# Kernel tuning notes

Hardware: AMD Instinct MI355X
Metric: run time of the kernel (lower is better)

Reference implementation:

```python
import jax, jax.numpy as jnp
import numpy as np

B, S, D, H = 1, 4096, 1024, 16
HD = D // H  # head_dim = 64
NEG = -1e9

def setup_inputs() -> dict:
    key = jax.random.key(0)
    ks = jax.random.split(key, 5)
    scale = 1.0 / np.sqrt(D)
    x = jax.random.normal(ks[0], (B, S, D), dtype=jnp.float32)
    Wq = jax.random.normal(ks[1], (D, D), dtype=jnp.float32) * scale
    Wk = jax.random.normal(ks[2], (D, D), dtype=jnp.float32) * scale
    Wv = jax.random.normal(ks[3], (D, D), dtype=jnp.float32) * scale
    Wo = jax.random.normal(ks[4], (D, D), dtype=jnp.float32) * scale
    mask = jnp.tril(jnp.ones((S, S), dtype=bool))[None, None]  # [1,1,S,S] causal
    return {"x": x, "mask": mask, "Wq": Wq, "Wk": Wk, "Wv": Wv, "Wo": Wo}

def reference(x, mask, Wq, Wk, Wv, Wo):
    # Linear projections (bias=False). nn.Linear computes x @ W.T; weights here
    # are stored as [out, in] so we use x @ W.T for faithfulness.
    q = x @ Wq.T  # [B,S,D]
    k = x @ Wk.T
    v = x @ Wv.T
    def split_heads(t):
        return t.reshape(B, S, H, HD).transpose(0, 2, 1, 3)  # [B,H,S,HD]
    q, k, v = split_heads(q), split_heads(k), split_heads(v)
    scores = jnp.einsum("bhqd,bhkd->bhqk", q, k) / jnp.sqrt(jnp.float32(HD))
    scores = jnp.where(mask, scores, NEG)
    attn = jax.nn.softmax(scores, axis=-1)  # dropout p=0.0 -> identity
    out = jnp.einsum("bhqk,bhkd->bhqd", attn, v)  # [B,H,S,HD]
    out = out.transpose(0, 2, 1, 3).reshape(B, S, D)
    return out @ Wo.T
```

## Files before the change

### kernel.cpp

```cpp
#include <hip/hip_runtime.h>
#include <hip/hip_bf16.h>


typedef __bf16 bf16x8 __attribute__((ext_vector_type(8)));
typedef __bf16 bf16x4 __attribute__((ext_vector_type(4)));
typedef float f32x4 __attribute__((ext_vector_type(4)));
typedef short s16x4 __attribute__((ext_vector_type(4)));

#define GAS __attribute__((address_space(1)))
#define LAS __attribute__((address_space(3)))

__device__ __forceinline__ void async_copy16(const void* g, void* l) {
  __builtin_amdgcn_global_load_lds((const GAS unsigned int*)g,
                                   (LAS unsigned int*)l, 16, 0, 0);
}

__device__ __forceinline__ f32x4 mfma_k16(bf16x4 a, bf16x4 b, f32x4 c) {
  union { bf16x4 h; s16x4 s; } ua, ub;
  ua.h = a; ub.h = b;
  return __builtin_amdgcn_mfma_f32_16x16x16bf16_1k(ua.s, ub.s, c, 0, 0, 0);
}

__global__ __launch_bounds__(256) void cvt_all(const float* __restrict__ x,
                                               const float* __restrict__ Wq,
                                               const float* __restrict__ Wk,
                                               const float* __restrict__ Wv,
                                               const float* __restrict__ Wo,
                                               __bf16* __restrict__ xb,
                                               __bf16* __restrict__ Wc,
                                               __bf16* __restrict__ Wob) {
  int b = blockIdx.x;
  const float* src;
  __bf16* dst;
  if (b < 4096)      { src = x  + (b       ) * 1024; dst = xb  + (long)b * 1024; }
  else if (b < 5120) { src = Wq + (b - 4096) * 1024; dst = Wc  + (long)(b - 4096) * 1024; }
  else if (b < 6144) { src = Wk + (b - 5120) * 1024; dst = Wc  + (1l << 20) + (long)(b - 5120) * 1024; }
  else if (b < 7168) { src = Wv + (b - 6144) * 1024; dst = Wc  + (2l << 20) + (long)(b - 6144) * 1024; }
  else               { src = Wo + (b - 7168) * 1024; dst = Wob + (long)(b - 7168) * 1024; }
  int i = threadIdx.x * 4;
  float4 f = *(const float4*)(src + i);
  bf16x4 o;
  o[0] = (__bf16)f.x; o[1] = (__bf16)f.y; o[2] = (__bf16)f.z; o[3] = (__bf16)f.w;
  *(bf16x4*)(dst + i) = o;
}

__global__ __launch_bounds__(256) void gemm_qkv(const __bf16* __restrict__ A,
                                                const __bf16* __restrict__ B,
                                                __bf16* __restrict__ Qb,
                                                __bf16* __restrict__ Kf,
                                                __bf16* __restrict__ Vf) {
  const int K = 1024;
  __shared__ __bf16 As[128 * 32];
  __shared__ __bf16 Bs[128 * 32];
  const int tid = threadIdx.x;
  const int lane = tid & 63, wv = tid >> 6;
  const int l15 = lane & 15, quad = lane >> 4;
  const int wm = wv >> 1, wn = wv & 1;
  const int mbase = blockIdx.y * 128, nbase = blockIdx.x * 128;
  const bool kswap = (nbase >= 1024) && (nbase < 2048);

  f32x4 acc[4][4] = {};

  for (int k0 = 0; k0 < K; k0 += 32) {
    __syncthreads();
#pragma unroll
    for (int q = 0; q < 2; ++q) {
      int i = q * 256 + tid;
      int row = i >> 2, kg = i & 3;
      const __bf16* ga = A + (long)(mbase + row) * K + k0 + kg * 8;
      const __bf16* gb = B + (long)(nbase + row) * K + k0 + kg * 8;
      char* la = (char*)As + (q * 256 + wv * 64) * 16;
      char* lb = (char*)Bs + (q * 256 + wv * 64) * 16;
      async_copy16(ga, la);
      async_copy16(gb, lb);
    }
    __syncthreads();
    bf16x8 af[4], bfr[4];
#pragma unroll
    for (int i = 0; i < 4; ++i)
      af[i] = *(const bf16x8*)&As[(wm * 64 + i * 16 + l15) * 32 + quad * 8];
#pragma unroll
    for (int j = 0; j < 4; ++j)
      bfr[j] = *(const bf16x8*)&Bs[(wn * 64 + j * 16 + l15) * 32 + quad * 8];
    if (kswap) {
#pragma unroll
      for (int i = 0; i < 4; ++i)
#pragma unroll
        for (int j = 0; j < 4; ++j)
          acc[i][j] = __builtin_amdgcn_mfma_f32_16x16x32_bf16(bfr[j], af[i], acc[i][j], 0, 0, 0);
    } else {
#pragma unroll
      for (int i = 0; i < 4; ++i)
#pragma unroll
        for (int j = 0; j < 4; ++j)
          acc[i][j] = __builtin_amdgcn_mfma_f32_16x16x32_bf16(af[i], bfr[j], acc[i][j], 0, 0, 0);
    }
  }

  if (nbase < 1024) {
    const float QS = 0.18033688011112043f;
#pragma unroll
    for (int i = 0; i < 4; ++i)
#pragma unroll
      for (int j = 0; j < 4; ++j) {
        int col = nbase + wn * 64 + j * 16 + l15;
#pragma unroll
        for (int r = 0; r < 4; ++r) {
          int row = mbase + wm * 64 + i * 16 + quad * 4 + r;
          Qb[(long)row * 1024 + col] = (__bf16)(acc[i][j][r] * QS);
        }
      }
  } else if (nbase < 2048) {
#pragma unroll
    for (int i = 0; i < 4; ++i)
#pragma unroll
      for (int j = 0; j < 4; ++j) {
        int d0 = nbase - 1024 + wn * 64 + j * 16 + quad * 4;
        int h = d0 >> 6, dd = d0 & 63;
        int kk = dd >> 5, qf = (dd >> 3) & 3, e0 = dd & 7;
        int kt = mbase + wm * 64 + i * 16 + l15;
        int tile = kt >> 6;
        long off = ((long)(h * 64 + tile) * 8 + i * 2 + kk) * 512 + (qf * 16 + l15) * 8 + e0;
        union { __bf16 b[4]; uint2 u; } pk;
#pragma unroll
        for (int r = 0; r < 4; ++r) pk.b[r] = (__bf16)acc[i][j][r];
        *(uint2*)(Kf + off) = pk.u;
      }
  } else {
#pragma unroll
    for (int i = 0; i < 4; ++i)
#pragma unroll
      for (int j = 0; j < 4; ++j) {
        int col = nbase - 2048 + wn * 64 + j * 16 + l15;
        int h = col >> 6, dd = col & 63;
        int jd = dd >> 4, lv = dd & 15;
        int kt0 = mbase + wm * 64 + i * 16 + quad * 4;
        int tile = kt0 >> 6, w6 = kt0 & 63;
        int jp = w6 >> 5, bit4 = (w6 >> 4) & 1, qv = (w6 >> 2) & 3;
        long off = ((long)(h * 64 + tile) * 8 + jd * 2 + jp) * 512 + (qv * 16 + lv) * 8 + bit4 * 4;
        union { __bf16 b[4]; uint2 u; } pk;
#pragma unroll
        for (int r = 0; r < 4; ++r) pk.b[r] = (__bf16)acc[i][j][r];
        *(uint2*)(Vf + off) = pk.u;
      }
  }
}

__global__ __launch_bounds__(256) void gemm_wo(const __bf16* __restrict__ A,
                                               const __bf16* __restrict__ B,
                                               float* __restrict__ C) {
  const int K = 1024, N = 1024;
  __shared__ __bf16 As[128 * 32];
  __shared__ __bf16 Bs[128 * 32];
  const int tid = threadIdx.x;
  const int lane = tid & 63, wv = tid >> 6;
  const int l15 = lane & 15, quad = lane >> 4;
  const int wm = wv >> 1, wn = wv & 1;
  const int mbase = blockIdx.y * 128, nbase = blockIdx.x * 128;

  f32x4 acc[4][4] = {};

  for (int k0 = 0; k0 < K; k0 += 32) {
    __syncthreads();
#pragma unroll
    for (int q = 0; q < 2; ++q) {
      int i = q * 256 + tid;
      int row = i >> 2, kg = i & 3;
      const __bf16* ga = A + (long)(mbase + row) * K + k0 + kg * 8;
      const __bf16* gb = B + (long)(nbase + row) * K + k0 + kg * 8;
      char* la = (char*)As + (q * 256 + wv * 64) * 16;
      char* lb = (char*)Bs + (q * 256 + wv * 64) * 16;
      async_copy16(ga, la);
      async_copy16(gb, lb);
    }
    __syncthreads();
    bf16x8 af[4], bfr[4];
#pragma unroll
    for (int i = 0; i < 4; ++i)
      af[i] = *(const bf16x8*)&As[(wm * 64 + i * 16 + l15) * 32 + quad * 8];
#pragma unroll
    for (int j = 0; j < 4; ++j)
      bfr[j] = *(const bf16x8*)&Bs[(wn * 64 + j * 16 + l15) * 32 + quad * 8];
#pragma unroll
    for (int i = 0; i < 4; ++i)
#pragma unroll
      for (int j = 0; j < 4; ++j)
        acc[i][j] = __builtin_amdgcn_mfma_f32_16x16x32_bf16(af[i], bfr[j], acc[i][j], 0, 0, 0);
  }
#pragma unroll
  for (int i = 0; i < 4; ++i)
#pragma unroll
    for (int j = 0; j < 4; ++j)
#pragma unroll
      for (int r = 0; r < 4; ++r) {
        int row = mbase + wm * 64 + i * 16 + quad * 4 + r;
        int col = nbase + wn * 64 + j * 16 + l15;
        C[(long)row * N + col] = acc[i][j][r];
      }
}

__global__ __launch_bounds__(512, 4) void flash_attn(const __bf16* __restrict__ Qb,
                                                     const __bf16* __restrict__ Kf,
                                                     const __bf16* __restrict__ Vf,
                                                     __bf16* __restrict__ AO) {
  const int tid = threadIdx.x;
  const int lane = tid & 63, l15 = lane & 15, quad = lane >> 4;
  const int w = tid >> 6;
  const int b = blockIdx.x;
  const int h = (b & 7) + 8 * ((b >> 3) & 1);
  const int g = b >> 4;
  const int p = g * 8 + w;
  const int hoff = h * 64;

  const __bf16* Kh = Kf + (long)h * 64 * 4096;
  const __bf16* Vh = Vf + (long)h * 64 * 4096;

#pragma unroll
  for (int pass = 0; pass < 2; ++pass) {
    const int t = pass ? (255 - p) : p;
    const int qrow = t * 16 + l15;
    bf16x8 qf[2];
    qf[0] = *(const bf16x8*)(Qb + (long)qrow * 1024 + hoff + quad * 8);
    qf[1] = *(const bf16x8*)(Qb + (long)qrow * 1024 + hoff + 32 + quad * 8);

    const int nkt = (t >> 2) + 1;
    f32x4 o_acc[4] = {};
    float l_acc = 0.0f;

    bf16x8 kc[8];
#pragma unroll
    for (int f = 0; f < 8; ++f)
      kc[f] = *(const bf16x8*)(Kh + f * 512 + lane * 8);

    for (int kt = 0; kt < nkt; ++kt) {
      const __bf16* Vt = Vh + (long)kt * 4096;

      bf16x8 va[8];
#pragma unroll
      for (int f = 0; f < 8; ++f)
        va[f] = *(const bf16x8*)(Vt + f * 512 + lane * 8);

      f32x4 st[4] = {};
#pragma unroll
      for (int j = 0; j < 4; ++j) {
        st[j] = __builtin_amdgcn_mfma_f32_16x16x32_bf16(kc[j * 2 + 0], qf[0], st[j], 0, 0, 0);
        st[j] = __builtin_amdgcn_mfma_f32_16x16x32_bf16(kc[j * 2 + 1], qf[1], st[j], 0, 0, 0);
      }

      if (kt + 1 < nkt) {
        const __bf16* Kt = Kh + (long)(kt + 1) * 4096;
#pragma unroll
        for (int f = 0; f < 8; ++f)
          kc[f] = *(const bf16x8*)(Kt + f * 512 + lane * 8);
      }

      if (kt == nkt - 1) {
        const int dq = (t & 3) * 16 + l15;
#pragma unroll
        for (int j = 0; j < 4; ++j)
#pragma unroll
          for (int r = 0; r < 4; ++r)
            if (j * 16 + quad * 4 + r > dq) st[j][r] = -3.0e38f;
      }

      bf16x4 pb[4];
      float ps = 0.0f;
#pragma unroll
      for (int j = 0; j < 4; ++j) {
        f32x4 pj;
#pragma unroll
        for (int r = 0; r < 4; ++r) pj[r] = __builtin_amdgcn_exp2f(st[j][r]);
        ps += (pj[0] + pj[1]) + (pj[2] + pj[3]);
        bf16x4 bb;
#pragma unroll
        for (int r = 0; r < 4; ++r) bb[r] = (__bf16)pj[r];
        pb[j] = bb;
      }
      l_acc += ps;

#pragma unroll
      for (int j = 0; j < 4; ++j) {
        bf16x4 pbj = pb[j];
#pragma unroll
        for (int jd = 0; jd < 4; ++jd) {
          bf16x8 v8 = va[jd * 2 + (j >> 1)];
          bf16x4 a4 = (j & 1) ? __builtin_shufflevector(v8, v8, 4, 5, 6, 7)
                              : __builtin_shufflevector(v8, v8, 0, 1, 2, 3);
          o_acc[jd] = mfma_k16(a4, pbj, o_acc[jd]);
        }
      }
    }

    l_acc += __shfl_xor(l_acc, 16);
    l_acc += __shfl_xor(l_acc, 32);
    const float inv = 1.0f / l_acc;

#pragma unroll
    for (int jd = 0; jd < 4; ++jd) {
      bf16x4 ob;
#pragma unroll
      for (int r = 0; r < 4; ++r) ob[r] = (__bf16)(o_acc[jd][r] * inv);
      *(bf16x4*)(AO + (long)qrow * 1024 + hoff + jd * 16 + quad * 4) = ob;
    }
  }
}

extern "C" void kernel_launch(void* const* d_in, const int* in_sizes, int n_in,
                              void* d_out, int out_size, void* d_ws, size_t ws_size,
                              hipStream_t stream) {
  const float* x  = (const float*)d_in[0];
  const float* Wq = (const float*)d_in[2];
  const float* Wk = (const float*)d_in[3];
  const float* Wv = (const float*)d_in[4];
  const float* Wo = (const float*)d_in[5];
  float* out = (float*)d_out;

  char* ws = (char*)d_ws;
  __bf16* xb  = (__bf16*)ws;
  __bf16* Wc  = (__bf16*)(ws + (8u << 20));
  __bf16* Wob = (__bf16*)(ws + (14u << 20));
  __bf16* Qb  = (__bf16*)(ws + (16u << 20));
  __bf16* Kfr = (__bf16*)(ws + (24u << 20));
  __bf16* Vfr = (__bf16*)(ws + (32u << 20));
  __bf16* AO  = (__bf16*)(ws + (40u << 20));

  cvt_all<<<8192, 256, 0, stream>>>(x, Wq, Wk, Wv, Wo, xb, Wc, Wob);

  dim3 g1(3072 / 128, 4096 / 128);
  gemm_qkv<<<g1, 256, 0, stream>>>(xb, Wc, Qb, Kfr, Vfr);

  flash_attn<<<256, 512, 0, stream>>>(Qb, Kfr, Vfr, AO);

  dim3 g2(1024 / 128, 4096 / 128);
  gemm_wo<<<g2, 256, 0, stream>>>(AO, Wob, out);
}
```

Measured before the change: 258.7 us.

## Split each query tile's key range across two waves and merge via LDS

```diff
diff --git a/kernel.cpp b/kernel.cpp
--- a/kernel.cpp
+++ b/kernel.cpp
@@ -203,13 +203,15 @@
                                                      const __bf16* __restrict__ Kf,
                                                      const __bf16* __restrict__ Vf,
                                                      __bf16* __restrict__ AO) {
+  __shared__ float Ms[4][64][17];
   const int tid = threadIdx.x;
   const int lane = tid & 63, l15 = lane & 15, quad = lane >> 4;
   const int w = tid >> 6;
+  const int pr = w >> 1, half = w & 1;
   const int b = blockIdx.x;
   const int h = (b & 7) + 8 * ((b >> 3) & 1);
   const int g = b >> 4;
-  const int p = g * 8 + w;
+  const int p = g * 4 + pr;
   const int hoff = h * 64;
 
   const __bf16* Kh = Kf + (long)h * 64 * 4096;
@@ -224,15 +226,20 @@
     qf[1] = *(const bf16x8*)(Qb + (long)qrow * 1024 + hoff + 32 + quad * 8);
 
     const int nkt = (t >> 2) + 1;
+    const int kt0 = half ? (nkt >> 1) : 0;
+    const int kt1 = half ? nkt : (nkt >> 1);
     f32x4 o_acc[4] = {};
     float l_acc = 0.0f;
 
     bf16x8 kc[8];
-#pragma unroll
-    for (int f = 0; f < 8; ++f)
-      kc[f] = *(const bf16x8*)(Kh + f * 512 + lane * 8);
-
-    for (int kt = 0; kt < nkt; ++kt) {
+    if (kt0 < kt1) {
+      const __bf16* Kt = Kh + (long)kt0 * 4096;
+#pragma unroll
+      for (int f = 0; f < 8; ++f)
+        kc[f] = *(const bf16x8*)(Kt + f * 512 + lane * 8);
+    }
+
+    for (int kt = kt0; kt < kt1; ++kt) {
       const __bf16* Vt = Vh + (long)kt * 4096;
 
       bf16x8 va[8];
@@ -247,7 +254,7 @@
         st[j] = __builtin_amdgcn_mfma_f32_16x16x32_bf16(kc[j * 2 + 1], qf[1], st[j], 0, 0, 0);
       }
 
-      if (kt + 1 < nkt) {
+      if (kt + 1 < kt1) {
         const __bf16* Kt = Kh + (long)(kt + 1) * 4096;
 #pragma unroll
         for (int f = 0; f < 8; ++f)
@@ -291,17 +298,36 @@
       }
     }
 
-    l_acc += __shfl_xor(l_acc, 16);
-    l_acc += __shfl_xor(l_acc, 32);
-    const float inv = 1.0f / l_acc;
-
-#pragma unroll
-    for (int jd = 0; jd < 4; ++jd) {
-      bf16x4 ob;
-#pragma unroll
-      for (int r = 0; r < 4; ++r) ob[r] = (__bf16)(o_acc[jd][r] * inv);
-      *(bf16x4*)(AO + (long)qrow * 1024 + hoff + jd * 16 + quad * 4) = ob;
-    }
+    if (half) {
+#pragma unroll
+      for (int jd = 0; jd < 4; ++jd)
+#pragma unroll
+        for (int r = 0; r < 4; ++r)
+          Ms[pr][lane][jd * 4 + r] = o_acc[jd][r];
+      Ms[pr][lane][16] = l_acc;
+    }
+    __syncthreads();
+    if (!half) {
+#pragma unroll
+      for (int jd = 0; jd < 4; ++jd)
+#pragma unroll
+        for (int r = 0; r < 4; ++r)
+          o_acc[jd][r] += Ms[pr][lane][jd * 4 + r];
+      l_acc += Ms[pr][lane][16];
+
+      l_acc += __shfl_xor(l_acc, 16);
+      l_acc += __shfl_xor(l_acc, 32);
+      const float inv = 1.0f / l_acc;
+
+#pragma unroll
+      for (int jd = 0; jd < 4; ++jd) {
+        bf16x4 ob;
+#pragma unroll
+        for (int r = 0; r < 4; ++r) ob[r] = (__bf16)(o_acc[jd][r] * inv);
+        *(bf16x4*)(AO + (long)qrow * 1024 + hoff + jd * 16 + quad * 4) = ob;
+      }
+    }
+    __syncthreads();
   }
 }
 
@@ -329,7 +355,7 @@
   dim3 g1(3072 / 128, 4096 / 128);
   gemm_qkv<<<g1, 256, 0, stream>>>(xb, Wc, Qb, Kfr, Vfr);
 
-  flash_attn<<<256, 512, 0, stream>>>(Qb, Kfr, Vfr, AO);
+  flash_attn<<<512, 512, 0, stream>>>(Qb, Kfr, Vfr, AO);
 
   dim3 g2(1024 / 128, 4096 / 128);
   gemm_wo<<<g2, 256, 0, stream>>>(AO, Wob, out);
```

Measured after the change: 257.9 us. No clear change (-0.3%).
